# Performance work log

Hardware: AMD Instinct MI355X
Metric: run time of the kernel (lower is better)

Reference implementation:

```python
import jax, jax.numpy as jnp
import numpy as np

B, H, Q, K, D = 2, 8, 512, 512, 64


def setup_inputs() -> dict:
    key = jax.random.key(0)
    ks = jax.random.split(key, 8)
    s = 1.0 / np.sqrt(D)
    return {
        "query": jax.random.normal(ks[0], (B, H, Q, D), dtype=jnp.float32),
        "keys": jax.random.normal(ks[1], (B, H, K, D), dtype=jnp.float32),
        "Wa_w": jax.random.normal(ks[2], (D, D), dtype=jnp.float32) * s,
        "Wa_b": jax.random.normal(ks[3], (D,), dtype=jnp.float32) * s,
        "Ua_w": jax.random.normal(ks[4], (D, D), dtype=jnp.float32) * s,
        "Ua_b": jax.random.normal(ks[5], (D,), dtype=jnp.float32) * s,
        "V_w": jax.random.normal(ks[6], (D,), dtype=jnp.float32) * s,
        "V_b": jax.random.normal(ks[7], (1,), dtype=jnp.float32) * s,
    }


def reference(query, keys, Wa_w, Wa_b, Ua_w, Ua_b, V_w, V_b):
    # Linear projections (torch Linear: x @ W.T + b)
    q_proj = jnp.einsum("bhqd,ed->bhqe", query, Wa_w) + Wa_b  # [B,H,Q,D]
    k_proj = jnp.einsum("bhkd,ed->bhke", keys, Ua_w) + Ua_b   # [B,H,K,D]
    # Broadcast add + tanh -> [B,H,Q,K,D] (the fusion-headroom intermediate)
    features = jnp.tanh(q_proj[:, :, :, None, :] + k_proj[:, :, None, :, :])
    # Linear reduce D -> scalar, squeeze last dim
    scores = jnp.einsum("bhqkd,d->bhqk", features, V_w) + V_b[0]  # [B,H,Q,K]
    return scores
```

## Files before the change

### kernel.cpp

```cpp
#include <hip/hip_runtime.h>


#define BHX 16
#define SEQ 512
#define DDIM 64
#define QT 32
#define KT 64

typedef float f4 __attribute__((ext_vector_type(4)));

__global__ __launch_bounds__(256) void proj_kernel(
    const float* __restrict__ query, const float* __restrict__ keys,
    const float* __restrict__ Wa_w,  const float* __restrict__ Wa_b,
    const float* __restrict__ Ua_w,  const float* __restrict__ Ua_b,
    float* __restrict__ eq, float* __restrict__ gk)
{
  const int t = threadIdx.x, lane = t & 63, wave = t >> 6;
  const bool is_k = blockIdx.x >= 256;
  const float* __restrict__ X  = is_k ? keys : query;
  const float* __restrict__ W  = is_k ? Ua_w : Wa_w;
  const float* __restrict__ Bv = is_k ? Ua_b : Wa_b;
  float* __restrict__ out      = is_k ? gk : eq;
  const int row0 = (blockIdx.x & 255) * 32;

  float w[64];
  const float4* W4 = (const float4*)(W + lane * DDIM);
#pragma unroll
  for (int i = 0; i < 16; ++i) {
    float4 v = W4[i];
    w[4*i] = v.x; w[4*i+1] = v.y; w[4*i+2] = v.z; w[4*i+3] = v.w;
  }

  const float C = 2.885390081777926815f;
  const float b = Bv[lane];

#pragma unroll 1
  for (int i = 0; i < 8; ++i) {
    const int r   = row0 + wave * 8 + i;
    const int off = __builtin_amdgcn_readfirstlane(r * DDIM);
    const float* xr = X + off;
    float a0 = 0, a1 = 0, a2 = 0, a3 = 0;
#pragma unroll
    for (int e = 0; e < 64; e += 4) {
      a0 = __builtin_fmaf(xr[e],     w[e],     a0);
      a1 = __builtin_fmaf(xr[e + 1], w[e + 1], a1);
      a2 = __builtin_fmaf(xr[e + 2], w[e + 2], a2);
      a3 = __builtin_fmaf(xr[e + 3], w[e + 3], a3);
    }
    float p = ((a0 + a1) + (a2 + a3)) + b;
    out[(size_t)r * DDIM + lane] = __builtin_amdgcn_exp2f(C * p);
  }
}

__global__ __launch_bounds__(256, 8) void score_kernel(
    const float* __restrict__ eq,
    const float* __restrict__ gk,
    const float* __restrict__ Vw,
    const float* __restrict__ Vb,
    float* __restrict__ out)
{
  __shared__ float ql[QT * DDIM];

  const int bh   = blockIdx.z;
  const int q0   = blockIdx.y * QT;
  const int k0   = blockIdx.x * KT;
  const int t    = threadIdx.x;
  const int lane = t & 63;
  const int wave = t >> 6;

  {
    const float4* src = (const float4*)(eq + (size_t)(bh * SEQ + q0) * DDIM);
    float4* dst = (float4*)ql;
    dst[t]       = src[t];
    dst[t + 256] = src[t + 256];
  }

  float acc0 = Vb[0];
#pragma unroll
  for (int d = 0; d < 64; ++d) acc0 += Vw[d];

  __syncthreads();

  float acc[8] = {0.f, 0.f, 0.f, 0.f, 0.f, 0.f, 0.f, 0.f};
  const int qrow0 = wave * 8;
  const float* gbase = gk + (size_t)(bh * SEQ + k0 + lane) * DDIM;

#pragma unroll 1
  for (int g = 0; g < 8; ++g) {
    const f4 G0 = *(const f4*)(gbase + 8 * g);
    const f4 G1 = *(const f4*)(gbase + 8 * g + 4);
    float vw[8];
#pragma unroll
    for (int j = 0; j < 8; ++j) vw[j] = Vw[8 * g + j];

#pragma unroll
    for (int qi = 0; qi < 8; ++qi) {
      const f4* ev = (const f4*)(ql + (qrow0 + qi) * DDIM + 8 * g);
      const f4 e0 = ev[0];
      const f4 e1 = ev[1];
      float A[8];
      A[0] = __builtin_fmaf(e0.x, G0.x, 1.0f);
      A[1] = __builtin_fmaf(e0.y, G0.y, 1.0f);
      A[2] = __builtin_fmaf(e0.z, G0.z, 1.0f);
      A[3] = __builtin_fmaf(e0.w, G0.w, 1.0f);
      A[4] = __builtin_fmaf(e1.x, G1.x, 1.0f);
      A[5] = __builtin_fmaf(e1.y, G1.y, 1.0f);
      A[6] = __builtin_fmaf(e1.z, G1.z, 1.0f);
      A[7] = __builtin_fmaf(e1.w, G1.w, 1.0f);
      const float n01 = __builtin_fmaf(vw[1], A[0], vw[0] * A[1]);
      const float n23 = __builtin_fmaf(vw[3], A[2], vw[2] * A[3]);
      const float n45 = __builtin_fmaf(vw[5], A[4], vw[4] * A[5]);
      const float n67 = __builtin_fmaf(vw[7], A[6], vw[6] * A[7]);
      const float P01 = A[0] * A[1], P23 = A[2] * A[3];
      const float P45 = A[4] * A[5], P67 = A[6] * A[7];
      const float n0123 = __builtin_fmaf(n23, P01, n01 * P23);
      const float n4567 = __builtin_fmaf(n67, P45, n45 * P67);
      const float P0123 = P01 * P23, P4567 = P45 * P67;
      const float num = __builtin_fmaf(n4567, P0123, n0123 * P4567);
      const float P   = P0123 * P4567;
      acc[qi] = __builtin_fmaf(num, __builtin_amdgcn_rcpf(P), acc[qi]);
    }
  }

  const size_t obase = (size_t)(bh * SEQ + q0 + qrow0) * SEQ + k0 + lane;
#pragma unroll
  for (int qi = 0; qi < 8; ++qi)
    out[obase + (size_t)qi * SEQ] = __builtin_fmaf(-2.f, acc[qi], acc0);
}

extern "C" void kernel_launch(void* const* d_in, const int* in_sizes, int n_in,
                              void* d_out, int out_size, void* d_ws, size_t ws_size,
                              hipStream_t stream) {
  const float* query = (const float*)d_in[0];
  const float* keys  = (const float*)d_in[1];
  const float* Wa_w  = (const float*)d_in[2];
  const float* Wa_b  = (const float*)d_in[3];
  const float* Ua_w  = (const float*)d_in[4];
  const float* Ua_b  = (const float*)d_in[5];
  const float* V_w   = (const float*)d_in[6];
  const float* V_b   = (const float*)d_in[7];
  float* out = (float*)d_out;

  const int R = BHX * SEQ;
  float* eq = (float*)d_ws;
  float* gk = eq + (size_t)R * DDIM;

  proj_kernel<<<512, 256, 0, stream>>>(query, keys, Wa_w, Wa_b,
                                       Ua_w, Ua_b, eq, gk);

  dim3 grid(SEQ / KT, SEQ / QT, BHX);
  score_kernel<<<grid, 256, 0, stream>>>(eq, gk, V_w, V_b, out);
}
```

Before: 47.52 us.

## Swap score tile roles: lanes over queries, keys read as wave-uniform loads

The score kernel's tile changes from 32 queries by 64 keys to 64 queries by 32 keys. Query exponentials are staged transposed in padded LDS, so each lane owns one query, and key rows are read through wave-uniform addresses that can become scalar loads. The output is then transposed through LDS and written with 16-byte coalesced stores. This is meant to take LDS reads out of the inner loop and replace per-lane vector global loads with broadcast loads, at the cost of an extra LDS round trip and two more barriers at the end.

```diff
diff --git a/kernel.cpp b/kernel.cpp
--- a/kernel.cpp
+++ b/kernel.cpp
@@ -4,8 +4,6 @@
 #define BHX 16
 #define SEQ 512
 #define DDIM 64
-#define QT 32
-#define KT 64
 
 typedef float f4 __attribute__((ext_vector_type(4)));
 
@@ -59,20 +57,28 @@
     const float* __restrict__ Vb,
     float* __restrict__ out)
 {
-  __shared__ float ql[QT * DDIM];
+  __shared__ float eql[DDIM][65];
 
   const int bh   = blockIdx.z;
-  const int q0   = blockIdx.y * QT;
-  const int k0   = blockIdx.x * KT;
+  const int q0   = blockIdx.y * 64;
+  const int k0   = blockIdx.x * 32;
   const int t    = threadIdx.x;
   const int lane = t & 63;
   const int wave = t >> 6;
 
   {
-    const float4* src = (const float4*)(eq + (size_t)(bh * SEQ + q0) * DDIM);
-    float4* dst = (float4*)ql;
-    dst[t]       = src[t];
-    dst[t + 256] = src[t + 256];
+    const float* eqb = eq + (size_t)(bh * SEQ + q0) * DDIM;
+#pragma unroll
+    for (int h = 0; h < 4; ++h) {
+      const int idx = t + 256 * h;
+      const int q   = idx >> 4;
+      const int d0  = (idx & 15) * 4;
+      const f4 v = *(const f4*)(eqb + q * DDIM + d0);
+      eql[d0][q]     = v.x;
+      eql[d0 + 1][q] = v.y;
+      eql[d0 + 2][q] = v.z;
+      eql[d0 + 3][q] = v.w;
+    }
   }
 
   float acc0 = Vb[0];
@@ -82,31 +88,24 @@
   __syncthreads();
 
   float acc[8] = {0.f, 0.f, 0.f, 0.f, 0.f, 0.f, 0.f, 0.f};
-  const int qrow0 = wave * 8;
-  const float* gbase = gk + (size_t)(bh * SEQ + k0 + lane) * DDIM;
+  const float* Gb = gk + (size_t)(bh * SEQ + k0 + wave * 8) * DDIM;
 
 #pragma unroll 1
   for (int g = 0; g < 8; ++g) {
-    const f4 G0 = *(const f4*)(gbase + 8 * g);
-    const f4 G1 = *(const f4*)(gbase + 8 * g + 4);
+    float e[8];
+#pragma unroll
+    for (int j = 0; j < 8; ++j) e[j] = eql[8 * g + j][lane];
     float vw[8];
 #pragma unroll
     for (int j = 0; j < 8; ++j) vw[j] = Vw[8 * g + j];
 
 #pragma unroll
-    for (int qi = 0; qi < 8; ++qi) {
-      const f4* ev = (const f4*)(ql + (qrow0 + qi) * DDIM + 8 * g);
-      const f4 e0 = ev[0];
-      const f4 e1 = ev[1];
+    for (int kk = 0; kk < 8; ++kk) {
+      const float* Gp = Gb + kk * DDIM + 8 * g;
       float A[8];
-      A[0] = __builtin_fmaf(e0.x, G0.x, 1.0f);
-      A[1] = __builtin_fmaf(e0.y, G0.y, 1.0f);
-      A[2] = __builtin_fmaf(e0.z, G0.z, 1.0f);
-      A[3] = __builtin_fmaf(e0.w, G0.w, 1.0f);
-      A[4] = __builtin_fmaf(e1.x, G1.x, 1.0f);
-      A[5] = __builtin_fmaf(e1.y, G1.y, 1.0f);
-      A[6] = __builtin_fmaf(e1.z, G1.z, 1.0f);
-      A[7] = __builtin_fmaf(e1.w, G1.w, 1.0f);
+#pragma unroll
+      for (int j = 0; j < 8; ++j)
+        A[j] = __builtin_fmaf(e[j], Gp[j], 1.0f);
       const float n01 = __builtin_fmaf(vw[1], A[0], vw[0] * A[1]);
       const float n23 = __builtin_fmaf(vw[3], A[2], vw[2] * A[3]);
       const float n45 = __builtin_fmaf(vw[5], A[4], vw[4] * A[5]);
@@ -118,14 +117,28 @@
       const float P0123 = P01 * P23, P4567 = P45 * P67;
       const float num = __builtin_fmaf(n4567, P0123, n0123 * P4567);
       const float P   = P0123 * P4567;
-      acc[qi] = __builtin_fmaf(num, __builtin_amdgcn_rcpf(P), acc[qi]);
+      acc[kk] = __builtin_fmaf(num, __builtin_amdgcn_rcpf(P), acc[kk]);
     }
   }
 
-  const size_t obase = (size_t)(bh * SEQ + q0 + qrow0) * SEQ + k0 + lane;
+  __syncthreads();
+  float* lo = &eql[0][0];
 #pragma unroll
-  for (int qi = 0; qi < 8; ++qi)
-    out[obase + (size_t)qi * SEQ] = __builtin_fmaf(-2.f, acc[qi], acc0);
+  for (int kk = 0; kk < 8; ++kk)
+    lo[lane * 33 + wave * 8 + kk] = __builtin_fmaf(-2.f, acc[kk], acc0);
+  __syncthreads();
+
+  {
+    const int row = t >> 2;
+    const int c0  = (t & 3) * 8;
+    const float* src = lo + row * 33 + c0;
+    f4 v0, v1;
+    v0.x = src[0]; v0.y = src[1]; v0.z = src[2]; v0.w = src[3];
+    v1.x = src[4]; v1.y = src[5]; v1.z = src[6]; v1.w = src[7];
+    float* dst = out + (size_t)(bh * SEQ + q0 + row) * SEQ + k0 + c0;
+    *(f4*)(dst)     = v0;
+    *(f4*)(dst + 4) = v1;
+  }
 }
 
 extern "C" void kernel_launch(void* const* d_in, const int* in_sizes, int n_in,
@@ -142,12 +155,12 @@
   float* out = (float*)d_out;
 
   const int R = BHX * SEQ;
-  float* eq = (float*)d_ws;
-  float* gk = eq + (size_t)R * DDIM;
+  float* eqw = (float*)d_ws;
+  float* gkw = eqw + (size_t)R * DDIM;
 
   proj_kernel<<<512, 256, 0, stream>>>(query, keys, Wa_w, Wa_b,
-                                       Ua_w, Ua_b, eq, gk);
+                                       Ua_w, Ua_b, eqw, gkw);
 
-  dim3 grid(SEQ / KT, SEQ / QT, BHX);
-  score_kernel<<<grid, 256, 0, stream>>>(eq, gk, V_w, V_b, out);
+  dim3 grid(SEQ / 32, SEQ / 64, BHX);
+  score_kernel<<<grid, 256, 0, stream>>>(eqw, gkw, V_w, V_b, out);
 }
```

Result: slower. 51.87 us (+9.2%).
